# Performance work log

Hardware: AMD Instinct MI355X
Metric: run time of the kernel (lower is better)

Reference implementation:

```python
import jax, jax.numpy as jnp
import numpy as np

N = 50000
H = 256
EPS = 1e-5

def setup_inputs() -> dict:
    key = jax.random.key(0)
    ks = jax.random.split(key, 8)
    d = 128
    inp = {
        'x': jax.random.normal(ks[0], (N, d), jnp.float32),
        'edge_index': jax.random.randint(ks[1], (2, 800000), 0, N, jnp.int64),
        'W1': jax.random.normal(ks[2], (d, H), jnp.float32) * (2.0 / d) ** 0.5,
        'b1': jnp.zeros((H,), jnp.float32),
        'g1': jnp.ones((H,), jnp.float32),
        'be1': jnp.zeros((H,), jnp.float32),
        'W2': jax.random.normal(ks[3], (H, H), jnp.float32) * (2.0 / H) ** 0.5,
        'b2': jnp.zeros((H,), jnp.float32),
        'g2': jnp.ones((H,), jnp.float32),
        'be2': jnp.zeros((H,), jnp.float32),
        'W3': jax.random.normal(ks[4], (H, H), jnp.float32) * (2.0 / H) ** 0.5,
        'b3': jnp.zeros((H,), jnp.float32),
        'g3': jnp.ones((H,), jnp.float32),
        'be3': jnp.zeros((H,), jnp.float32),
        'Wf1': jax.random.normal(ks[5], (H, H // 2), jnp.float32) * (2.0 / H) ** 0.5,
        'bf1': jnp.zeros((H // 2,), jnp.float32),
        'Wf2': jax.random.normal(ks[6], (H // 2, 1), jnp.float32) * (2.0 / (H // 2)) ** 0.5,
        'bf2': jnp.zeros((1,), jnp.float32),
    }
    return inp

def _gcn_norm(edge_index):
    # add self-loops, symmetric normalization (PyG GCNConv defaults)
    loop = jnp.arange(N, dtype=edge_index.dtype)
    row = jnp.concatenate([edge_index[0], loop])  # source
    col = jnp.concatenate([edge_index[1], loop])  # target
    deg = jax.ops.segment_sum(jnp.ones_like(col, jnp.float32), col, num_segments=N)
    dis = jnp.where(deg > 0, jax.lax.rsqrt(deg), 0.0)
    norm = dis[row] * dis[col]  # [E+N]
    return row, col, norm

def _conv(x, W, b, row, col, norm):
    xw = x @ W                       # [N,H]
    msg = xw[row] * norm[:, None]    # gather + scale, [E+N,H]
    out = jax.ops.segment_sum(msg, col, num_segments=N)
    return out + b

def _ln(x, g, b):
    mu = jnp.mean(x, axis=-1, keepdims=True)
    var = jnp.var(x, axis=-1, keepdims=True)
    return (x - mu) * jax.lax.rsqrt(var + EPS) * g + b

def reference(x, edge_index, W1, b1, g1, be1, W2, b2, g2, be2, W3, b3, g3, be3, Wf1, bf1, Wf2, bf2):
    row, col, norm = _gcn_norm(edge_index)
    x1 = jax.nn.relu(_ln(_conv(x, W1, b1, row, col, norm), g1, be1))
    x2 = jax.nn.relu(_ln(_conv(x1, W2, b2, row, col, norm), g2, be2)) + 0.7 * x1
    x3 = jax.nn.relu(_ln(_conv(x2, W3, b3, row, col, norm), g3, be3)) * 0.7 + x2
    h = jax.nn.relu(x3 @ Wf1 + bf1)
    return h @ Wf2 + bf2  # [N,1]
```

## Files before the change

kernel.cpp:

```cpp
#include <hip/hip_runtime.h>
#include <cstdint>
#include <cstddef>

#define HDIM 256
#define DIN 128
#define EPSV 1e-5f
#define SCHUNK 1024

typedef __attribute__((ext_vector_type(8))) short short8;
typedef __attribute__((ext_vector_type(4))) float f32x4;

__device__ __forceinline__ float bf2f(unsigned int u16) {
  union { unsigned int i; float f; } v; v.i = u16 << 16; return v.f;
}
__device__ __forceinline__ unsigned short f2bf(float f) {
  union { float f; unsigned int i; } v; v.f = f;
  unsigned int u = v.i;
  return (unsigned short)((u + 0x7fffu + ((u >> 16) & 1u)) >> 16);
}
__device__ __forceinline__ float4 ldbf4(const unsigned short* p) {
  uint2 v = *(const uint2*)p;
  return make_float4(bf2f(v.x & 0xffffu), bf2f(v.x >> 16),
                     bf2f(v.y & 0xffffu), bf2f(v.y >> 16));
}
__device__ __forceinline__ void stbf4(unsigned short* p, float a, float b, float c, float d) {
  uint2 o;
  o.x = (unsigned int)f2bf(a) | ((unsigned int)f2bf(b) << 16);
  o.y = (unsigned int)f2bf(c) | ((unsigned int)f2bf(d) << 16);
  *(uint2*)p = o;
}
#define ACC8(u) do { \
    acc[0] += bf2f((u).x & 0xffffu); acc[1] += bf2f((u).x >> 16); \
    acc[2] += bf2f((u).y & 0xffffu); acc[3] += bf2f((u).y >> 16); \
    acc[4] += bf2f((u).z & 0xffffu); acc[5] += bf2f((u).z >> 16); \
    acc[6] += bf2f((u).w & 0xffffu); acc[7] += bf2f((u).w >> 16); } while (0)

__global__ __launch_bounds__(256) void hist_k(const int* __restrict__ col, int* deg, int e) {
  int i = blockIdx.x * 256 + threadIdx.x;
  if (i < e) atomicAdd(&deg[col[i]], 1);
}

__global__ __launch_bounds__(256) void scanA_k(const int* __restrict__ deg,
                                               int* __restrict__ row_ptr,
                                               int* __restrict__ blockSums,
                                               float* __restrict__ dis, int n) {
  __shared__ int waveSums[4];
  const int tid = threadIdx.x, lane = tid & 63, w = tid >> 6;
  const int base = blockIdx.x * SCHUNK + tid * 4;
  int v0 = 0, v1 = 0, v2 = 0, v3 = 0;
  if (base + 0 < n) v0 = deg[base + 0];
  if (base + 1 < n) v1 = deg[base + 1];
  if (base + 2 < n) v2 = deg[base + 2];
  if (base + 3 < n) v3 = deg[base + 3];
  if (base + 0 < n) dis[base + 0] = rsqrtf((float)(v0 + 1));
  if (base + 1 < n) dis[base + 1] = rsqrtf((float)(v1 + 1));
  if (base + 2 < n) dis[base + 2] = rsqrtf((float)(v2 + 1));
  if (base + 3 < n) dis[base + 3] = rsqrtf((float)(v3 + 1));
  int tsum = v0 + v1 + v2 + v3;
  int inc = tsum;
#pragma unroll
  for (int off = 1; off < 64; off <<= 1) {
    int t = __shfl_up(inc, off);
    if (lane >= off) inc += t;
  }
  if (lane == 63) waveSums[w] = inc;
  __syncthreads();
  int woff = 0;
#pragma unroll
  for (int k = 0; k < 4; ++k) woff += (k < w) ? waveSums[k] : 0;
  int excl = woff + inc - tsum;
  if (base + 0 < n) row_ptr[base + 0] = excl;
  if (base + 1 < n) row_ptr[base + 1] = excl + v0;
  if (base + 2 < n) row_ptr[base + 2] = excl + v0 + v1;
  if (base + 3 < n) row_ptr[base + 3] = excl + v0 + v1 + v2;
  if (tid == 255) blockSums[blockIdx.x] = woff + inc;
}

__global__ __launch_bounds__(256) void scanC_k(int* __restrict__ row_ptr,
                                               const int* __restrict__ bsums,
                                               int n, int e, int nbs) {
  __shared__ int s_add;
  if (threadIdx.x < 64) {
    int v = (threadIdx.x < nbs && threadIdx.x < blockIdx.x) ? bsums[threadIdx.x] : 0;
#pragma unroll
    for (int off = 1; off < 64; off <<= 1) v += __shfl_xor(v, off);
    if (threadIdx.x == 0) s_add = v;
  }
  __syncthreads();
  const int add = s_add;
  const int base = blockIdx.x * SCHUNK + threadIdx.x * 4;
#pragma unroll
  for (int k = 0; k < 4; ++k)
    if (base + k < n) row_ptr[base + k] += add;
  if (blockIdx.x == 0 && threadIdx.x == 0) row_ptr[n] = e;
}

__global__ __launch_bounds__(256) void fill_k(const int* __restrict__ row,
                                              const int* __restrict__ col,
                                              const int* __restrict__ row_ptr,
                                              int* cur, int* srcs, int e) {
  int i = blockIdx.x * 256 + threadIdx.x;
  if (i < e) {
    int c = col[i];
    int p = row_ptr[c] + atomicAdd(&cur[c], 1);
    srcs[p] = row[i];
  }
}

__device__ __forceinline__ void packW(const float* __restrict__ W,
                                      unsigned short* __restrict__ out,
                                      int idx, int C) {
  int j = idx & 7, lane = (idx >> 3) & 63, rest = idx >> 9;
  int NSUB = C >> 4;
  int ns = rest % NSUB, kb = rest / NSUB;
  int k = kb * 32 + (lane >> 4) * 8 + j;
  int c = ns * 16 + (lane & 15);
  out[idx] = f2bf(W[(size_t)k * C + c]);
}

__global__ __launch_bounds__(256) void prep_k(
    const float* __restrict__ W1, const float* __restrict__ W2,
    const float* __restrict__ W3, const float* __restrict__ Wf1,
    const float* __restrict__ x, const float* __restrict__ dis,
    unsigned short* __restrict__ W1p, unsigned short* __restrict__ W2p,
    unsigned short* __restrict__ W3p, unsigned short* __restrict__ Wf1p,
    unsigned short* __restrict__ xs, int nx) {
  int idx = blockIdx.x * 256 + threadIdx.x;
  const int s0 = DIN * HDIM, s1 = s0 + HDIM * HDIM, s2 = s1 + HDIM * HDIM,
            s3 = s2 + HDIM * 128;
  if (idx < s0) packW(W1, W1p, idx, HDIM);
  else if (idx < s1) packW(W2, W2p, idx - s0, HDIM);
  else if (idx < s2) packW(W3, W3p, idx - s1, HDIM);
  else if (idx < s3) packW(Wf1, Wf1p, idx - s2, 128);
  else {
    int o = idx - s3;
    if (o < nx) xs[o] = f2bf(x[o] * dis[o >> 7]);
  }
}

__global__ __launch_bounds__(256) void gather256_k(
    const unsigned short* __restrict__ xs, const int* __restrict__ row_ptr,
    const int* __restrict__ srcs, const float* __restrict__ dis,
    unsigned short* __restrict__ out, int n) {
  int wv = blockIdx.x * 4 + (threadIdx.x >> 6);
  int lane = threadIdx.x & 63;
  int half = lane >> 5, li = lane & 31;
  int i = wv * 2 + half;
  bool valid = i < n;
  int ic = valid ? i : n - 1;
  int beg = row_ptr[ic], end = row_ptr[ic + 1];
  float di = dis[ic];
  const int co = li * 8;
  const unsigned short* xb = xs + co;
  float acc[8];
  {
    uint4 v = *(const uint4*)(xb + (size_t)ic * 256);
    acc[0] = bf2f(v.x & 0xffffu); acc[1] = bf2f(v.x >> 16);
    acc[2] = bf2f(v.y & 0xffffu); acc[3] = bf2f(v.y >> 16);
    acc[4] = bf2f(v.z & 0xffffu); acc[5] = bf2f(v.z >> 16);
    acc[6] = bf2f(v.w & 0xffffu); acc[7] = bf2f(v.w >> 16);
  }
  int j = beg;
  for (; j + 16 <= end; j += 16) {
    int4 sA = *(const int4*)(srcs + j);
    int4 sB = *(const int4*)(srcs + j + 4);
    int4 sC = *(const int4*)(srcs + j + 8);
    int4 sD = *(const int4*)(srcs + j + 12);
    uint4 u0 = *(const uint4*)(xb + (size_t)sA.x * 256);
    uint4 u1 = *(const uint4*)(xb + (size_t)sA.y * 256);
    uint4 u2 = *(const uint4*)(xb + (size_t)sA.z * 256);
    uint4 u3 = *(const uint4*)(xb + (size_t)sA.w * 256);
    uint4 u4 = *(const uint4*)(xb + (size_t)sB.x * 256);
    uint4 u5 = *(const uint4*)(xb + (size_t)sB.y * 256);
    uint4 u6 = *(const uint4*)(xb + (size_t)sB.z * 256);
    uint4 u7 = *(const uint4*)(xb + (size_t)sB.w * 256);
    uint4 u8 = *(const uint4*)(xb + (size_t)sC.x * 256);
    uint4 u9 = *(const uint4*)(xb + (size_t)sC.y * 256);
    uint4 uA = *(const uint4*)(xb + (size_t)sC.z * 256);
    uint4 uB = *(const uint4*)(xb + (size_t)sC.w * 256);
    uint4 uC = *(const uint4*)(xb + (size_t)sD.x * 256);
    uint4 uD = *(const uint4*)(xb + (size_t)sD.y * 256);
    uint4 uE = *(const uint4*)(xb + (size_t)sD.z * 256);
    uint4 uF = *(const uint4*)(xb + (size_t)sD.w * 256);
    ACC8(u0); ACC8(u1); ACC8(u2); ACC8(u3);
    ACC8(u4); ACC8(u5); ACC8(u6); ACC8(u7);
    ACC8(u8); ACC8(u9); ACC8(uA); ACC8(uB);
    ACC8(uC); ACC8(uD); ACC8(uE); ACC8(uF);
  }
  for (; j + 4 <= end; j += 4) {
    int4 sA = *(const int4*)(srcs + j);
    uint4 u0 = *(const uint4*)(xb + (size_t)sA.x * 256);
    uint4 u1 = *(const uint4*)(xb + (size_t)sA.y * 256);
    uint4 u2 = *(const uint4*)(xb + (size_t)sA.z * 256);
    uint4 u3 = *(const uint4*)(xb + (size_t)sA.w * 256);
    ACC8(u0); ACC8(u1); ACC8(u2); ACC8(u3);
  }
  for (; j < end; ++j) {
    uint4 u = *(const uint4*)(xb + (size_t)srcs[j] * 256);
    ACC8(u);
  }
  if (valid) {
    uint4 o;
    o.x = (unsigned int)f2bf(di * acc[0]) | ((unsigned int)f2bf(di * acc[1]) << 16);
    o.y = (unsigned int)f2bf(di * acc[2]) | ((unsigned int)f2bf(di * acc[3]) << 16);
    o.z = (unsigned int)f2bf(di * acc[4]) | ((unsigned int)f2bf(di * acc[5]) << 16);
    o.w = (unsigned int)f2bf(di * acc[6]) | ((unsigned int)f2bf(di * acc[7]) << 16);
    *(uint4*)(out + (size_t)i * 256 + co) = o;
  }
}

__global__ __launch_bounds__(256) void gather128_k(
    const unsigned short* __restrict__ xs, const int* __restrict__ row_ptr,
    const int* __restrict__ srcs, const float* __restrict__ dis,
    unsigned short* __restrict__ out, int n) {
  int wv = blockIdx.x * 4 + (threadIdx.x >> 6);
  int lane = threadIdx.x & 63;
  int q = lane >> 4, li = lane & 15;
  int i = wv * 4 + q;
  bool valid = i < n;
  int ic = valid ? i : n - 1;
  int beg = row_ptr[ic], end = row_ptr[ic + 1];
  float di = dis[ic];
  const int co = li * 8;
  const unsigned short* xb = xs + co;
  float acc[8];
  {
    uint4 v = *(const uint4*)(xb + (size_t)ic * 128);
    acc[0] = bf2f(v.x & 0xffffu); acc[1] = bf2f(v.x >> 16);
    acc[2] = bf2f(v.y & 0xffffu); acc[3] = bf2f(v.y >> 16);
    acc[4] = bf2f(v.z & 0xffffu); acc[5] = bf2f(v.z >> 16);
    acc[6] = bf2f(v.w & 0xffffu); acc[7] = bf2f(v.w >> 16);
  }
  int j = beg;
  for (; j + 16 <= end; j += 16) {
    int4 sA = *(const int4*)(srcs + j);
    int4 sB = *(const int4*)(srcs + j + 4);
    int4 sC = *(const int4*)(srcs + j + 8);
    int4 sD = *(const int4*)(srcs + j + 12);
    uint4 u0 = *(const uint4*)(xb + (size_t)sA.x * 128);
    uint4 u1 = *(const uint4*)(xb + (size_t)sA.y * 128);
    uint4 u2 = *(const uint4*)(xb + (size_t)sA.z * 128);
    uint4 u3 = *(const uint4*)(xb + (size_t)sA.w * 128);
    uint4 u4 = *(const uint4*)(xb + (size_t)sB.x * 128);
    uint4 u5 = *(const uint4*)(xb + (size_t)sB.y * 128);
    uint4 u6 = *(const uint4*)(xb + (size_t)sB.z * 128);
    uint4 u7 = *(const uint4*)(xb + (size_t)sB.w * 128);
    uint4 u8 = *(const uint4*)(xb + (size_t)sC.x * 128);
    uint4 u9 = *(const uint4*)(xb + (size_t)sC.y * 128);
    uint4 uA = *(const uint4*)(xb + (size_t)sC.z * 128);
    uint4 uB = *(const uint4*)(xb + (size_t)sC.w * 128);
    uint4 uC = *(const uint4*)(xb + (size_t)sD.x * 128);
    uint4 uD = *(const uint4*)(xb + (size_t)sD.y * 128);
    uint4 uE = *(const uint4*)(xb + (size_t)sD.z * 128);
    uint4 uF = *(const uint4*)(xb + (size_t)sD.w * 128);
    ACC8(u0); ACC8(u1); ACC8(u2); ACC8(u3);
    ACC8(u4); ACC8(u5); ACC8(u6); ACC8(u7);
    ACC8(u8); ACC8(u9); ACC8(uA); ACC8(uB);
    ACC8(uC); ACC8(uD); ACC8(uE); ACC8(uF);
  }
  for (; j + 4 <= end; j += 4) {
    int4 sA = *(const int4*)(srcs + j);
    uint4 u0 = *(const uint4*)(xb + (size_t)sA.x * 128);
    uint4 u1 = *(const uint4*)(xb + (size_t)sA.y * 128);
    uint4 u2 = *(const uint4*)(xb + (size_t)sA.z * 128);
    uint4 u3 = *(const uint4*)(xb + (size_t)sA.w * 128);
    ACC8(u0); ACC8(u1); ACC8(u2); ACC8(u3);
  }
  for (; j < end; ++j) {
    uint4 u = *(const uint4*)(xb + (size_t)srcs[j] * 128);
    ACC8(u);
  }
  if (valid) {
    uint4 o;
    o.x = (unsigned int)f2bf(di * acc[0]) | ((unsigned int)f2bf(di * acc[1]) << 16);
    o.y = (unsigned int)f2bf(di * acc[2]) | ((unsigned int)f2bf(di * acc[3]) << 16);
    o.z = (unsigned int)f2bf(di * acc[4]) | ((unsigned int)f2bf(di * acc[5]) << 16);
    o.w = (unsigned int)f2bf(di * acc[6]) | ((unsigned int)f2bf(di * acc[7]) << 16);
    *(uint4*)(out + (size_t)i * 128 + co) = o;
  }
}

template<int MODE, int K, bool SOUT>
__global__ __launch_bounds__(512) void gemmln_k(
    const unsigned short* __restrict__ A, const unsigned short* __restrict__ Wp,
    const float* __restrict__ bias, const float* __restrict__ gam,
    const float* __restrict__ bet, const unsigned short* __restrict__ xprev,
    const float* __restrict__ dis, unsigned short* __restrict__ out, int n) {
  constexpr int CN = 256, NSUB = 16, KC = K / 32;
  __shared__ float red_s[64][4], red_q[64][4];
  const int t = threadIdx.x;
  const int w = t >> 6, lane = t & 63;
  const int rg = w & 1, cg = w >> 1;
  const int gq = lane >> 4, i = lane & 15;
  const int m0 = blockIdx.x * 64;
  const int r0 = m0 + rg * 32 + i, r1 = r0 + 16;
  const int l0 = r0 < n ? r0 : n - 1, l1 = r1 < n ? r1 : n - 1;
  const unsigned short* a0 = A + (size_t)l0 * K + gq * 8;
  const unsigned short* a1 = A + (size_t)l1 * K + gq * 8;
  const short8* wp = (const short8*)Wp + (size_t)(cg * 4) * 64 + lane;

  f32x4 acc[2][4];
#pragma unroll
  for (int rr = 0; rr < 2; ++rr)
#pragma unroll
    for (int j = 0; j < 4; ++j) acc[rr][j] = (f32x4){0.f, 0.f, 0.f, 0.f};

  short8 af0 = *(const short8*)a0;
  short8 af1 = *(const short8*)a1;
  short8 wf[4];
#pragma unroll
  for (int j = 0; j < 4; ++j) wf[j] = wp[j * 64];

#pragma unroll
  for (int kc = 0; kc < KC; ++kc) {
    short8 naf0, naf1, nwf[4];
    if (kc + 1 < KC) {
      naf0 = *(const short8*)(a0 + (kc + 1) * 32);
      naf1 = *(const short8*)(a1 + (kc + 1) * 32);
#pragma unroll
      for (int j = 0; j < 4; ++j) nwf[j] = wp[(size_t)(kc + 1) * NSUB * 64 + j * 64];
    }
#pragma unroll
    for (int j = 0; j < 4; ++j) {
      acc[0][j] = __builtin_amdgcn_mfma_f32_16x16x32_bf16(wf[j], af0, acc[0][j], 0, 0, 0);
      acc[1][j] = __builtin_amdgcn_mfma_f32_16x16x32_bf16(wf[j], af1, acc[1][j], 0, 0, 0);
    }
    if (kc + 1 < KC) {
      af0 = naf0; af1 = naf1;
#pragma unroll
      for (int j = 0; j < 4; ++j) wf[j] = nwf[j];
    }
  }

  const int colb = cg * 64 + gq * 4;
  float s0 = 0.f, q0 = 0.f, s1 = 0.f, q1 = 0.f;
#pragma unroll
  for (int j = 0; j < 4; ++j) {
    f32x4 b4 = *(const f32x4*)(bias + colb + j * 16);
#pragma unroll
    for (int r = 0; r < 4; ++r) {
      acc[0][j][r] += b4[r];
      acc[1][j][r] += b4[r];
      float v = acc[0][j][r]; s0 += v; q0 += v * v;
      float u = acc[1][j][r]; s1 += u; q1 += u * u;
    }
  }
  s0 += __shfl_xor(s0, 16); s0 += __shfl_xor(s0, 32);
  q0 += __shfl_xor(q0, 16); q0 += __shfl_xor(q0, 32);
  s1 += __shfl_xor(s1, 16); s1 += __shfl_xor(s1, 32);
  q1 += __shfl_xor(q1, 16); q1 += __shfl_xor(q1, 32);
  if (gq == 0) {
    red_s[rg * 32 + i][cg] = s0;      red_q[rg * 32 + i][cg] = q0;
    red_s[rg * 32 + 16 + i][cg] = s1; red_q[rg * 32 + 16 + i][cg] = q1;
  }
  __syncthreads();

#pragma unroll
  for (int rr = 0; rr < 2; ++rr) {
    int il = rg * 32 + rr * 16 + i;
    int r = m0 + il;
    if (r >= n) continue;
    float ss = (red_s[il][0] + red_s[il][1]) + (red_s[il][2] + red_s[il][3]);
    float qq = (red_q[il][0] + red_q[il][1]) + (red_q[il][2] + red_q[il][3]);
    float mu = ss * (1.f / CN);
    float inv = rsqrtf(qq * (1.f / CN) - mu * mu + EPSV);
    float di = dis[r];
    float rinv = (MODE != 0) ? 1.0f / di : 0.f;
    unsigned short* op = out + (size_t)r * CN + colb;
    const unsigned short* pp = (MODE != 0) ? (xprev + (size_t)r * CN + colb) : nullptr;
#pragma unroll
    for (int j = 0; j < 4; ++j) {
      f32x4 g4 = *(const f32x4*)(gam + colb + j * 16);
      f32x4 e4 = *(const f32x4*)(bet + colb + j * 16);
      float o0 = fmaxf((acc[rr][j][0] - mu) * inv * g4[0] + e4[0], 0.f);
      float o1 = fmaxf((acc[rr][j][1] - mu) * inv * g4[1] + e4[1], 0.f);
      float o2 = fmaxf((acc[rr][j][2] - mu) * inv * g4[2] + e4[2], 0.f);
      float o3 = fmaxf((acc[rr][j][3] - mu) * inv * g4[3] + e4[3], 0.f);
      if (MODE == 1) {
        float4 pv = ldbf4(pp + j * 16);
        o0 += 0.7f * rinv * pv.x; o1 += 0.7f * rinv * pv.y;
        o2 += 0.7f * rinv * pv.z; o3 += 0.7f * rinv * pv.w;
      } else if (MODE == 2) {
        float4 pv = ldbf4(pp + j * 16);
        o0 = o0 * 0.7f + rinv * pv.x; o1 = o1 * 0.7f + rinv * pv.y;
        o2 = o2 * 0.7f + rinv * pv.z; o3 = o3 * 0.7f + rinv * pv.w;
      }
      if (SOUT) { o0 *= di; o1 *= di; o2 *= di; o3 *= di; }
      stbf4(op + j * 16, o0, o1, o2, o3);
    }
  }
}

__global__ __launch_bounds__(256) void gemmdot_k(
    const unsigned short* __restrict__ A, const unsigned short* __restrict__ Wp,
    const float* __restrict__ b1, const float* __restrict__ w2,
    const float* __restrict__ b2, float* __restrict__ out, int n) {
  constexpr int K = 256, NSUB = 8, KC = 8;
  __shared__ float redh[64][2];
  const int t = threadIdx.x;
  const int w = t >> 6, lane = t & 63;
  const int rg = w & 1, cg = w >> 1;
  const int gq = lane >> 4, i = lane & 15;
  const int m0 = blockIdx.x * 64;
  const int r0 = m0 + rg * 32 + i, r1 = r0 + 16;
  const int l0 = r0 < n ? r0 : n - 1, l1 = r1 < n ? r1 : n - 1;
  const unsigned short* a0 = A + (size_t)l0 * K + gq * 8;
  const unsigned short* a1 = A + (size_t)l1 * K + gq * 8;
  const short8* wp = (const short8*)Wp + (size_t)(cg * 4) * 64 + lane;

  f32x4 acc[2][4];
#pragma unroll
  for (int rr = 0; rr < 2; ++rr)
#pragma unroll
    for (int j = 0; j < 4; ++j) acc[rr][j] = (f32x4){0.f, 0.f, 0.f, 0.f};

  short8 af0 = *(const short8*)a0;
  short8 af1 = *(const short8*)a1;
  short8 wf[4];
#pragma unroll
  for (int j = 0; j < 4; ++j) wf[j] = wp[j * 64];

#pragma unroll
  for (int kc = 0; kc < KC; ++kc) {
    short8 naf0, naf1, nwf[4];
    if (kc + 1 < KC) {
      naf0 = *(const short8*)(a0 + (kc + 1) * 32);
      naf1 = *(const short8*)(a1 + (kc + 1) * 32);
#pragma unroll
      for (int j = 0; j < 4; ++j) nwf[j] = wp[(size_t)(kc + 1) * NSUB * 64 + j * 64];
    }
#pragma unroll
    for (int j = 0; j < 4; ++j) {
      acc[0][j] = __builtin_amdgcn_mfma_f32_16x16x32_bf16(wf[j], af0, acc[0][j], 0, 0, 0);
      acc[1][j] = __builtin_amdgcn_mfma_f32_16x16x32_bf16(wf[j], af1, acc[1][j], 0, 0, 0);
    }
    if (kc + 1 < KC) {
      af0 = naf0; af1 = naf1;
#pragma unroll
      for (int j = 0; j < 4; ++j) wf[j] = nwf[j];
    }
  }

  const int colb = cg * 64 + gq * 4;
  float p0 = 0.f, p1 = 0.f;
#pragma unroll
  for (int j = 0; j < 4; ++j) {
    f32x4 bb = *(const f32x4*)(b1 + colb + j * 16);
    f32x4 ww = *(const f32x4*)(w2 + colb + j * 16);
#pragma unroll
    for (int r = 0; r < 4; ++r) {
      p0 += fmaxf(acc[0][j][r] + bb[r], 0.f) * ww[r];
      p1 += fmaxf(acc[1][j][r] + bb[r], 0.f) * ww[r];
    }
  }
  p0 += __shfl_xor(p0, 16); p0 += __shfl_xor(p0, 32);
  p1 += __shfl_xor(p1, 16); p1 += __shfl_xor(p1, 32);
  if (gq == 0) {
    redh[rg * 32 + i][cg] = p0;
    redh[rg * 32 + 16 + i][cg] = p1;
  }
  __syncthreads();
  if (t < 64) {
    int r = m0 + t;
    if (r < n) out[r] = redh[t][0] + redh[t][1] + b2[0];
  }
}

extern "C" void kernel_launch(void* const* d_in, const int* in_sizes, int n_in,
                              void* d_out, int out_size, void* d_ws, size_t ws_size,
                              hipStream_t stream) {
  const float* x   = (const float*)d_in[0];
  const int*   ei  = (const int*)d_in[1];
  const float* W1  = (const float*)d_in[2];
  const float* b1  = (const float*)d_in[3];
  const float* g1  = (const float*)d_in[4];
  const float* be1 = (const float*)d_in[5];
  const float* W2  = (const float*)d_in[6];
  const float* b2  = (const float*)d_in[7];
  const float* g2  = (const float*)d_in[8];
  const float* be2 = (const float*)d_in[9];
  const float* W3  = (const float*)d_in[10];
  const float* b3  = (const float*)d_in[11];
  const float* g3  = (const float*)d_in[12];
  const float* be3 = (const float*)d_in[13];
  const float* Wf1 = (const float*)d_in[14];
  const float* bf1 = (const float*)d_in[15];
  const float* Wf2 = (const float*)d_in[16];
  const float* bf2 = (const float*)d_in[17];
  float* out = (float*)d_out;

  const int n = in_sizes[0] / DIN;
  const int e = in_sizes[1] / 2;
  const int* row = ei;
  const int* col = ei + e;

  char* ws = (char*)d_ws;
  size_t off = 0;
  auto alloc = [&](size_t bytes) -> void* {
    void* p = ws + off;
    off = (off + bytes + 255) & ~(size_t)255;
    return p;
  };
  float*          dis     = (float*)alloc((size_t)n * 4);
  int*            deg_i   = (int*)alloc((size_t)n * 4);
  int*            cur     = (int*)alloc((size_t)n * 4);
  int*            row_ptr = (int*)alloc((size_t)(n + 1) * 4);
  int*            bsums   = (int*)alloc((size_t)256 * 4);
  int*            srcs    = (int*)alloc((size_t)e * 4);
  unsigned short* W1p     = (unsigned short*)alloc((size_t)DIN * HDIM * 2);
  unsigned short* W2p     = (unsigned short*)alloc((size_t)HDIM * HDIM * 2);
  unsigned short* W3p     = (unsigned short*)alloc((size_t)HDIM * HDIM * 2);
  unsigned short* Wf1p    = (unsigned short*)alloc((size_t)HDIM * 128 * 2);
  unsigned short* xsb     = (unsigned short*)alloc((size_t)n * DIN * 2);
  unsigned short* agg     = (unsigned short*)alloc((size_t)n * HDIM * 2);
  unsigned short* x1s     = (unsigned short*)alloc((size_t)n * HDIM * 2);
  unsigned short* x2s     = (unsigned short*)alloc((size_t)n * HDIM * 2);
  unsigned short* a1      = agg;
  unsigned short* x3      = x1s;

  const int eb  = (e + 255) / 256;
  const int gb  = (n + 63) / 64;
  const int sb_ = (n + SCHUNK - 1) / SCHUNK;
  const int g2b = (n + 7) / 8;
  const int g1b = (n + 15) / 16;
  const int prep_tot = DIN * HDIM + HDIM * HDIM + HDIM * HDIM + HDIM * 128 + n * DIN;

  hipMemsetAsync(deg_i, 0, ((char*)row_ptr - (char*)deg_i), stream);
  hist_k<<<eb, 256, 0, stream>>>(col, deg_i, e);
  scanA_k<<<sb_, 256, 0, stream>>>(deg_i, row_ptr, bsums, dis, n);
  scanC_k<<<sb_, 256, 0, stream>>>(row_ptr, bsums, n, e, sb_);
  fill_k<<<eb, 256, 0, stream>>>(row, col, row_ptr, cur, srcs, e);

  prep_k<<<(prep_tot + 255) / 256, 256, 0, stream>>>(W1, W2, W3, Wf1, x, dis,
                                                     W1p, W2p, W3p, Wf1p, xsb, n * DIN);

  gather128_k<<<g1b, 256, 0, stream>>>(xsb, row_ptr, srcs, dis, a1, n);
  gemmln_k<0, DIN, true><<<gb, 512, 0, stream>>>(a1, W1p, b1, g1, be1, nullptr, dis, x1s, n);

  gather256_k<<<g2b, 256, 0, stream>>>(x1s, row_ptr, srcs, dis, agg, n);
  gemmln_k<1, HDIM, true><<<gb, 512, 0, stream>>>(agg, W2p, b2, g2, be2, x1s, dis, x2s, n);

  gather256_k<<<g2b, 256, 0, stream>>>(x2s, row_ptr, srcs, dis, agg, n);
  gemmln_k<2, HDIM, false><<<gb, 512, 0, stream>>>(agg, W3p, b3, g3, be3, x2s, dis, x3, n);

  gemmdot_k<<<gb, 256, 0, stream>>>(x3, Wf1p, bf1, Wf2, bf2, out, n);
}
```

Before: 470.5 us.

## Fuse neighbor gather into GEMM+LayerNorm kernel via shared-memory tile

```diff
diff --git a/kernel.cpp b/kernel.cpp
--- a/kernel.cpp
+++ b/kernel.cpp
@@ -138,165 +138,97 @@
   }
 }
 
-__global__ __launch_bounds__(256) void gather256_k(
+template<int MODE, int K, bool SOUT>
+__global__ __launch_bounds__(512) void fused_k(
     const unsigned short* __restrict__ xs, const int* __restrict__ row_ptr,
     const int* __restrict__ srcs, const float* __restrict__ dis,
-    unsigned short* __restrict__ out, int n) {
-  int wv = blockIdx.x * 4 + (threadIdx.x >> 6);
-  int lane = threadIdx.x & 63;
-  int half = lane >> 5, li = lane & 31;
-  int i = wv * 2 + half;
-  bool valid = i < n;
-  int ic = valid ? i : n - 1;
-  int beg = row_ptr[ic], end = row_ptr[ic + 1];
-  float di = dis[ic];
-  const int co = li * 8;
-  const unsigned short* xb = xs + co;
-  float acc[8];
-  {
-    uint4 v = *(const uint4*)(xb + (size_t)ic * 256);
-    acc[0] = bf2f(v.x & 0xffffu); acc[1] = bf2f(v.x >> 16);
-    acc[2] = bf2f(v.y & 0xffffu); acc[3] = bf2f(v.y >> 16);
-    acc[4] = bf2f(v.z & 0xffffu); acc[5] = bf2f(v.z >> 16);
-    acc[6] = bf2f(v.w & 0xffffu); acc[7] = bf2f(v.w >> 16);
-  }
-  int j = beg;
-  for (; j + 16 <= end; j += 16) {
-    int4 sA = *(const int4*)(srcs + j);
-    int4 sB = *(const int4*)(srcs + j + 4);
-    int4 sC = *(const int4*)(srcs + j + 8);
-    int4 sD = *(const int4*)(srcs + j + 12);
-    uint4 u0 = *(const uint4*)(xb + (size_t)sA.x * 256);
-    uint4 u1 = *(const uint4*)(xb + (size_t)sA.y * 256);
-    uint4 u2 = *(const uint4*)(xb + (size_t)sA.z * 256);
-    uint4 u3 = *(const uint4*)(xb + (size_t)sA.w * 256);
-    uint4 u4 = *(const uint4*)(xb + (size_t)sB.x * 256);
-    uint4 u5 = *(const uint4*)(xb + (size_t)sB.y * 256);
-    uint4 u6 = *(const uint4*)(xb + (size_t)sB.z * 256);
-    uint4 u7 = *(const uint4*)(xb + (size_t)sB.w * 256);
-    uint4 u8 = *(const uint4*)(xb + (size_t)sC.x * 256);
-    uint4 u9 = *(const uint4*)(xb + (size_t)sC.y * 256);
-    uint4 uA = *(const uint4*)(xb + (size_t)sC.z * 256);
-    uint4 uB = *(const uint4*)(xb + (size_t)sC.w * 256);
-    uint4 uC = *(const uint4*)(xb + (size_t)sD.x * 256);
-    uint4 uD = *(const uint4*)(xb + (size_t)sD.y * 256);
-    uint4 uE = *(const uint4*)(xb + (size_t)sD.z * 256);
-    uint4 uF = *(const uint4*)(xb + (size_t)sD.w * 256);
-    ACC8(u0); ACC8(u1); ACC8(u2); ACC8(u3);
-    ACC8(u4); ACC8(u5); ACC8(u6); ACC8(u7);
-    ACC8(u8); ACC8(u9); ACC8(uA); ACC8(uB);
-    ACC8(uC); ACC8(uD); ACC8(uE); ACC8(uF);
-  }
-  for (; j + 4 <= end; j += 4) {
-    int4 sA = *(const int4*)(srcs + j);
-    uint4 u0 = *(const uint4*)(xb + (size_t)sA.x * 256);
-    uint4 u1 = *(const uint4*)(xb + (size_t)sA.y * 256);
-    uint4 u2 = *(const uint4*)(xb + (size_t)sA.z * 256);
-    uint4 u3 = *(const uint4*)(xb + (size_t)sA.w * 256);
-    ACC8(u0); ACC8(u1); ACC8(u2); ACC8(u3);
-  }
-  for (; j < end; ++j) {
-    uint4 u = *(const uint4*)(xb + (size_t)srcs[j] * 256);
-    ACC8(u);
-  }
-  if (valid) {
-    uint4 o;
-    o.x = (unsigned int)f2bf(di * acc[0]) | ((unsigned int)f2bf(di * acc[1]) << 16);
-    o.y = (unsigned int)f2bf(di * acc[2]) | ((unsigned int)f2bf(di * acc[3]) << 16);
-    o.z = (unsigned int)f2bf(di * acc[4]) | ((unsigned int)f2bf(di * acc[5]) << 16);
-    o.w = (unsigned int)f2bf(di * acc[6]) | ((unsigned int)f2bf(di * acc[7]) << 16);
-    *(uint4*)(out + (size_t)i * 256 + co) = o;
-  }
-}
-
-__global__ __launch_bounds__(256) void gather128_k(
-    const unsigned short* __restrict__ xs, const int* __restrict__ row_ptr,
-    const int* __restrict__ srcs, const float* __restrict__ dis,
-    unsigned short* __restrict__ out, int n) {
-  int wv = blockIdx.x * 4 + (threadIdx.x >> 6);
-  int lane = threadIdx.x & 63;
-  int q = lane >> 4, li = lane & 15;
-  int i = wv * 4 + q;
-  bool valid = i < n;
-  int ic = valid ? i : n - 1;
-  int beg = row_ptr[ic], end = row_ptr[ic + 1];
-  float di = dis[ic];
-  const int co = li * 8;
-  const unsigned short* xb = xs + co;
-  float acc[8];
-  {
-    uint4 v = *(const uint4*)(xb + (size_t)ic * 128);
-    acc[0] = bf2f(v.x & 0xffffu); acc[1] = bf2f(v.x >> 16);
-    acc[2] = bf2f(v.y & 0xffffu); acc[3] = bf2f(v.y >> 16);
-    acc[4] = bf2f(v.z & 0xffffu); acc[5] = bf2f(v.z >> 16);
-    acc[6] = bf2f(v.w & 0xffffu); acc[7] = bf2f(v.w >> 16);
-  }
-  int j = beg;
-  for (; j + 16 <= end; j += 16) {
-    int4 sA = *(const int4*)(srcs + j);
-    int4 sB = *(const int4*)(srcs + j + 4);
-    int4 sC = *(const int4*)(srcs + j + 8);
-    int4 sD = *(const int4*)(srcs + j + 12);
-    uint4 u0 = *(const uint4*)(xb + (size_t)sA.x * 128);
-    uint4 u1 = *(const uint4*)(xb + (size_t)sA.y * 128);
-    uint4 u2 = *(const uint4*)(xb + (size_t)sA.z * 128);
-    uint4 u3 = *(const uint4*)(xb + (size_t)sA.w * 128);
-    uint4 u4 = *(const uint4*)(xb + (size_t)sB.x * 128);
-    uint4 u5 = *(const uint4*)(xb + (size_t)sB.y * 128);
-    uint4 u6 = *(const uint4*)(xb + (size_t)sB.z * 128);
-    uint4 u7 = *(const uint4*)(xb + (size_t)sB.w * 128);
-    uint4 u8 = *(const uint4*)(xb + (size_t)sC.x * 128);
-    uint4 u9 = *(const uint4*)(xb + (size_t)sC.y * 128);
-    uint4 uA = *(const uint4*)(xb + (size_t)sC.z * 128);
-    uint4 uB = *(const uint4*)(xb + (size_t)sC.w * 128);
-    uint4 uC = *(const uint4*)(xb + (size_t)sD.x * 128);
-    uint4 uD = *(const uint4*)(xb + (size_t)sD.y * 128);
-    uint4 uE = *(const uint4*)(xb + (size_t)sD.z * 128);
-    uint4 uF = *(const uint4*)(xb + (size_t)sD.w * 128);
-    ACC8(u0); ACC8(u1); ACC8(u2); ACC8(u3);
-    ACC8(u4); ACC8(u5); ACC8(u6); ACC8(u7);
-    ACC8(u8); ACC8(u9); ACC8(uA); ACC8(uB);
-    ACC8(uC); ACC8(uD); ACC8(uE); ACC8(uF);
-  }
-  for (; j + 4 <= end; j += 4) {
-    int4 sA = *(const int4*)(srcs + j);
-    uint4 u0 = *(const uint4*)(xb + (size_t)sA.x * 128);
-    uint4 u1 = *(const uint4*)(xb + (size_t)sA.y * 128);
-    uint4 u2 = *(const uint4*)(xb + (size_t)sA.z * 128);
-    uint4 u3 = *(const uint4*)(xb + (size_t)sA.w * 128);
-    ACC8(u0); ACC8(u1); ACC8(u2); ACC8(u3);
-  }
-  for (; j < end; ++j) {
-    uint4 u = *(const uint4*)(xb + (size_t)srcs[j] * 128);
-    ACC8(u);
-  }
-  if (valid) {
-    uint4 o;
-    o.x = (unsigned int)f2bf(di * acc[0]) | ((unsigned int)f2bf(di * acc[1]) << 16);
-    o.y = (unsigned int)f2bf(di * acc[2]) | ((unsigned int)f2bf(di * acc[3]) << 16);
-    o.z = (unsigned int)f2bf(di * acc[4]) | ((unsigned int)f2bf(di * acc[5]) << 16);
-    o.w = (unsigned int)f2bf(di * acc[6]) | ((unsigned int)f2bf(di * acc[7]) << 16);
-    *(uint4*)(out + (size_t)i * 128 + co) = o;
-  }
-}
-
-template<int MODE, int K, bool SOUT>
-__global__ __launch_bounds__(512) void gemmln_k(
-    const unsigned short* __restrict__ A, const unsigned short* __restrict__ Wp,
+    const unsigned short* __restrict__ Wp,
     const float* __restrict__ bias, const float* __restrict__ gam,
     const float* __restrict__ bet, const unsigned short* __restrict__ xprev,
-    const float* __restrict__ dis, unsigned short* __restrict__ out, int n) {
+    unsigned short* __restrict__ out, int n) {
   constexpr int CN = 256, NSUB = 16, KC = K / 32;
+  constexpr int STRIDE = K + 8;
+  constexpr int LPR = K / 8;
+  constexpr int RP = 64 / LPR;
+  constexpr int NIT = 8 / RP;
+  __shared__ unsigned short aggS[64 * STRIDE];
   __shared__ float red_s[64][4], red_q[64][4];
+
   const int t = threadIdx.x;
   const int w = t >> 6, lane = t & 63;
+  const int m0 = blockIdx.x * 64;
+
+  {
+    const int gi = lane / LPR, li = lane % LPR;
+    const unsigned short* xb = xs + li * 8;
+#pragma unroll
+    for (int it = 0; it < NIT; ++it) {
+      const int lr = w * 8 + it * RP + gi;
+      const int tg = m0 + lr;
+      const int tgc = tg < n ? tg : n - 1;
+      const int beg = row_ptr[tgc], end = row_ptr[tgc + 1];
+      const float di = dis[tgc];
+      float acc[8];
+      {
+        uint4 v = *(const uint4*)(xb + (size_t)tgc * K);
+        acc[0] = bf2f(v.x & 0xffffu); acc[1] = bf2f(v.x >> 16);
+        acc[2] = bf2f(v.y & 0xffffu); acc[3] = bf2f(v.y >> 16);
+        acc[4] = bf2f(v.z & 0xffffu); acc[5] = bf2f(v.z >> 16);
+        acc[6] = bf2f(v.w & 0xffffu); acc[7] = bf2f(v.w >> 16);
+      }
+      int j = beg;
+      for (; j + 16 <= end; j += 16) {
+        int4 sA = *(const int4*)(srcs + j);
+        int4 sB = *(const int4*)(srcs + j + 4);
+        int4 sC = *(const int4*)(srcs + j + 8);
+        int4 sD = *(const int4*)(srcs + j + 12);
+        uint4 u0 = *(const uint4*)(xb + (size_t)sA.x * K);
+        uint4 u1 = *(const uint4*)(xb + (size_t)sA.y * K);
+        uint4 u2 = *(const uint4*)(xb + (size_t)sA.z * K);
+        uint4 u3 = *(const uint4*)(xb + (size_t)sA.w * K);
+        uint4 u4 = *(const uint4*)(xb + (size_t)sB.x * K);
+        uint4 u5 = *(const uint4*)(xb + (size_t)sB.y * K);
+        uint4 u6 = *(const uint4*)(xb + (size_t)sB.z * K);
+        uint4 u7 = *(const uint4*)(xb + (size_t)sB.w * K);
+        uint4 u8 = *(const uint4*)(xb + (size_t)sC.x * K);
+        uint4 u9 = *(const uint4*)(xb + (size_t)sC.y * K);
+        uint4 uA = *(const uint4*)(xb + (size_t)sC.z * K);
+        uint4 uB = *(const uint4*)(xb + (size_t)sC.w * K);
+        uint4 uC = *(const uint4*)(xb + (size_t)sD.x * K);
+        uint4 uD = *(const uint4*)(xb + (size_t)sD.y * K);
+        uint4 uE = *(const uint4*)(xb + (size_t)sD.z * K);
+        uint4 uF = *(const uint4*)(xb + (size_t)sD.w * K);
+        ACC8(u0); ACC8(u1); ACC8(u2); ACC8(u3);
+        ACC8(u4); ACC8(u5); ACC8(u6); ACC8(u7);
+        ACC8(u8); ACC8(u9); ACC8(uA); ACC8(uB);
+        ACC8(uC); ACC8(uD); ACC8(uE); ACC8(uF);
+      }
+      for (; j + 4 <= end; j += 4) {
+        int4 sA = *(const int4*)(srcs + j);
+        uint4 u0 = *(const uint4*)(xb + (size_t)sA.x * K);
+        uint4 u1 = *(const uint4*)(xb + (size_t)sA.y * K);
+        uint4 u2 = *(const uint4*)(xb + (size_t)sA.z * K);
+        uint4 u3 = *(const uint4*)(xb + (size_t)sA.w * K);
+        ACC8(u0); ACC8(u1); ACC8(u2); ACC8(u3);
+      }
+      for (; j < end; ++j) {
+        uint4 u = *(const uint4*)(xb + (size_t)srcs[j] * K);
+        ACC8(u);
+      }
+      uint4 o;
+      o.x = (unsigned int)f2bf(di * acc[0]) | ((unsigned int)f2bf(di * acc[1]) << 16);
+      o.y = (unsigned int)f2bf(di * acc[2]) | ((unsigned int)f2bf(di * acc[3]) << 16);
+      o.z = (unsigned int)f2bf(di * acc[4]) | ((unsigned int)f2bf(di * acc[5]) << 16);
+      o.w = (unsigned int)f2bf(di * acc[6]) | ((unsigned int)f2bf(di * acc[7]) << 16);
+      *(uint4*)&aggS[lr * STRIDE + li * 8] = o;
+    }
+  }
+  __syncthreads();
+
   const int rg = w & 1, cg = w >> 1;
   const int gq = lane >> 4, i = lane & 15;
-  const int m0 = blockIdx.x * 64;
-  const int r0 = m0 + rg * 32 + i, r1 = r0 + 16;
-  const int l0 = r0 < n ? r0 : n - 1, l1 = r1 < n ? r1 : n - 1;
-  const unsigned short* a0 = A + (size_t)l0 * K + gq * 8;
-  const unsigned short* a1 = A + (size_t)l1 * K + gq * 8;
+  const unsigned short* aL0 = &aggS[(rg * 32 + i) * STRIDE + gq * 8];
+  const unsigned short* aL1 = aL0 + 16 * STRIDE;
   const short8* wp = (const short8*)Wp + (size_t)(cg * 4) * 64 + lane;
 
   f32x4 acc[2][4];
@@ -305,28 +237,25 @@
 #pragma unroll
     for (int j = 0; j < 4; ++j) acc[rr][j] = (f32x4){0.f, 0.f, 0.f, 0.f};
 
-  short8 af0 = *(const short8*)a0;
-  short8 af1 = *(const short8*)a1;
   short8 wf[4];
 #pragma unroll
   for (int j = 0; j < 4; ++j) wf[j] = wp[j * 64];
 
 #pragma unroll
   for (int kc = 0; kc < KC; ++kc) {
-    short8 naf0, naf1, nwf[4];
+    short8 nwf[4];
     if (kc + 1 < KC) {
-      naf0 = *(const short8*)(a0 + (kc + 1) * 32);
-      naf1 = *(const short8*)(a1 + (kc + 1) * 32);
 #pragma unroll
       for (int j = 0; j < 4; ++j) nwf[j] = wp[(size_t)(kc + 1) * NSUB * 64 + j * 64];
     }
+    short8 af0 = *(const short8*)(aL0 + kc * 32);
+    short8 af1 = *(const short8*)(aL1 + kc * 32);
 #pragma unroll
     for (int j = 0; j < 4; ++j) {
       acc[0][j] = __builtin_amdgcn_mfma_f32_16x16x32_bf16(wf[j], af0, acc[0][j], 0, 0, 0);
       acc[1][j] = __builtin_amdgcn_mfma_f32_16x16x32_bf16(wf[j], af1, acc[1][j], 0, 0, 0);
     }
     if (kc + 1 < KC) {
-      af0 = naf0; af1 = naf1;
 #pragma unroll
       for (int j = 0; j < 4; ++j) wf[j] = nwf[j];
     }
@@ -512,17 +441,13 @@
   unsigned short* W3p     = (unsigned short*)alloc((size_t)HDIM * HDIM * 2);
   unsigned short* Wf1p    = (unsigned short*)alloc((size_t)HDIM * 128 * 2);
   unsigned short* xsb     = (unsigned short*)alloc((size_t)n * DIN * 2);
-  unsigned short* agg     = (unsigned short*)alloc((size_t)n * HDIM * 2);
   unsigned short* x1s     = (unsigned short*)alloc((size_t)n * HDIM * 2);
   unsigned short* x2s     = (unsigned short*)alloc((size_t)n * HDIM * 2);
-  unsigned short* a1      = agg;
-  unsigned short* x3      = x1s;
+  unsigned short* x3      = (unsigned short*)alloc((size_t)n * HDIM * 2);
 
   const int eb  = (e + 255) / 256;
   const int gb  = (n + 63) / 64;
   const int sb_ = (n + SCHUNK - 1) / SCHUNK;
-  const int g2b = (n + 7) / 8;
-  const int g1b = (n + 15) / 16;
   const int prep_tot = DIN * HDIM + HDIM * HDIM + HDIM * HDIM + HDIM * 128 + n * DIN;
 
   hipMemsetAsync(deg_i, 0, ((char*)row_ptr - (char*)deg_i), stream);
@@ -534,14 +459,14 @@
   prep_k<<<(prep_tot + 255) / 256, 256, 0, stream>>>(W1, W2, W3, Wf1, x, dis,
                                                      W1p, W2p, W3p, Wf1p, xsb, n * DIN);
 
-  gather128_k<<<g1b, 256, 0, stream>>>(xsb, row_ptr, srcs, dis, a1, n);
-  gemmln_k<0, DIN, true><<<gb, 512, 0, stream>>>(a1, W1p, b1, g1, be1, nullptr, dis, x1s, n);
-
-  gather256_k<<<g2b, 256, 0, stream>>>(x1s, row_ptr, srcs, dis, agg, n);
-  gemmln_k<1, HDIM, true><<<gb, 512, 0, stream>>>(agg, W2p, b2, g2, be2, x1s, dis, x2s, n);
-
-  gather256_k<<<g2b, 256, 0, stream>>>(x2s, row_ptr, srcs, dis, agg, n);
-  gemmln_k<2, HDIM, false><<<gb, 512, 0, stream>>>(agg, W3p, b3, g3, be3, x2s, dis, x3, n);
+  fused_k<0, DIN, true><<<gb, 512, 0, stream>>>(
+      xsb, row_ptr, srcs, dis, W1p, b1, g1, be1, nullptr, x1s, n);
+
+  fused_k<1, HDIM, true><<<gb, 512, 0, stream>>>(
+      x1s, row_ptr, srcs, dis, W2p, b2, g2, be2, x1s, x2s, n);
+
+  fused_k<2, HDIM, false><<<gb, 512, 0, stream>>>(
+      x2s, row_ptr, srcs, dis, W3p, b3, g3, be3, x2s, x3, n);
 
   gemmdot_k<<<gb, 256, 0, stream>>>(x3, Wf1p, bf1, Wf2, bf2, out, n);
 }
```

After: 480.4 us. +2.1%, slower.

## Widen GEMM tiles to 128 rows and record atomic ranks in CSR build

Applied to the files above, without the earlier changes.

```diff
diff --git a/kernel.cpp b/kernel.cpp
--- a/kernel.cpp
+++ b/kernel.cpp
@@ -35,9 +35,10 @@
     acc[4] += bf2f((u).z & 0xffffu); acc[5] += bf2f((u).z >> 16); \
     acc[6] += bf2f((u).w & 0xffffu); acc[7] += bf2f((u).w >> 16); } while (0)
 
-__global__ __launch_bounds__(256) void hist_k(const int* __restrict__ col, int* deg, int e) {
+__global__ __launch_bounds__(256) void hist_k(const int* __restrict__ col,
+                                              int* deg, int* __restrict__ rank, int e) {
   int i = blockIdx.x * 256 + threadIdx.x;
-  if (i < e) atomicAdd(&deg[col[i]], 1);
+  if (i < e) rank[i] = atomicAdd(&deg[col[i]], 1);
 }
 
 __global__ __launch_bounds__(256) void scanA_k(const int* __restrict__ deg,
@@ -98,13 +99,10 @@
 __global__ __launch_bounds__(256) void fill_k(const int* __restrict__ row,
                                               const int* __restrict__ col,
                                               const int* __restrict__ row_ptr,
-                                              int* cur, int* srcs, int e) {
+                                              const int* __restrict__ rank,
+                                              int* __restrict__ srcs, int e) {
   int i = blockIdx.x * 256 + threadIdx.x;
-  if (i < e) {
-    int c = col[i];
-    int p = row_ptr[c] + atomicAdd(&cur[c], 1);
-    srcs[p] = row[i];
-  }
+  if (i < e) srcs[row_ptr[col[i]] + rank[i]] = row[i];
 }
 
 __device__ __forceinline__ void packW(const float* __restrict__ W,
@@ -286,56 +284,56 @@
     const float* __restrict__ bias, const float* __restrict__ gam,
     const float* __restrict__ bet, const unsigned short* __restrict__ xprev,
     const float* __restrict__ dis, unsigned short* __restrict__ out, int n) {
-  constexpr int CN = 256, NSUB = 16, KC = K / 32;
-  __shared__ float red_s[64][4], red_q[64][4];
+  constexpr int CN = 256, NSUBT = 16, KC = K / 32;
+  __shared__ float red_s[128][2], red_q[128][2];
   const int t = threadIdx.x;
   const int w = t >> 6, lane = t & 63;
-  const int rg = w & 1, cg = w >> 1;
+  const int rg = w & 3, cg = w >> 2;
   const int gq = lane >> 4, i = lane & 15;
-  const int m0 = blockIdx.x * 64;
+  const int m0 = blockIdx.x * 128;
   const int r0 = m0 + rg * 32 + i, r1 = r0 + 16;
   const int l0 = r0 < n ? r0 : n - 1, l1 = r1 < n ? r1 : n - 1;
   const unsigned short* a0 = A + (size_t)l0 * K + gq * 8;
   const unsigned short* a1 = A + (size_t)l1 * K + gq * 8;
-  const short8* wp = (const short8*)Wp + (size_t)(cg * 4) * 64 + lane;
-
-  f32x4 acc[2][4];
+  const short8* wp = (const short8*)Wp + (size_t)(cg * 8) * 64 + lane;
+
+  f32x4 acc[2][8];
 #pragma unroll
   for (int rr = 0; rr < 2; ++rr)
 #pragma unroll
-    for (int j = 0; j < 4; ++j) acc[rr][j] = (f32x4){0.f, 0.f, 0.f, 0.f};
+    for (int j = 0; j < 8; ++j) acc[rr][j] = (f32x4){0.f, 0.f, 0.f, 0.f};
 
   short8 af0 = *(const short8*)a0;
   short8 af1 = *(const short8*)a1;
-  short8 wf[4];
-#pragma unroll
-  for (int j = 0; j < 4; ++j) wf[j] = wp[j * 64];
+  short8 wf[8];
+#pragma unroll
+  for (int j = 0; j < 8; ++j) wf[j] = wp[j * 64];
 
 #pragma unroll
   for (int kc = 0; kc < KC; ++kc) {
-    short8 naf0, naf1, nwf[4];
+    short8 naf0, naf1, nwf[8];
     if (kc + 1 < KC) {
       naf0 = *(const short8*)(a0 + (kc + 1) * 32);
       naf1 = *(const short8*)(a1 + (kc + 1) * 32);
 #pragma unroll
-      for (int j = 0; j < 4; ++j) nwf[j] = wp[(size_t)(kc + 1) * NSUB * 64 + j * 64];
-    }
-#pragma unroll
-    for (int j = 0; j < 4; ++j) {
+      for (int j = 0; j < 8; ++j) nwf[j] = wp[(size_t)(kc + 1) * NSUBT * 64 + j * 64];
+    }
+#pragma unroll
+    for (int j = 0; j < 8; ++j) {
       acc[0][j] = __builtin_amdgcn_mfma_f32_16x16x32_bf16(wf[j], af0, acc[0][j], 0, 0, 0);
       acc[1][j] = __builtin_amdgcn_mfma_f32_16x16x32_bf16(wf[j], af1, acc[1][j], 0, 0, 0);
     }
     if (kc + 1 < KC) {
       af0 = naf0; af1 = naf1;
 #pragma unroll
-      for (int j = 0; j < 4; ++j) wf[j] = nwf[j];
-    }
-  }
-
-  const int colb = cg * 64 + gq * 4;
+      for (int j = 0; j < 8; ++j) wf[j] = nwf[j];
+    }
+  }
+
+  const int colb = cg * 128 + gq * 4;
   float s0 = 0.f, q0 = 0.f, s1 = 0.f, q1 = 0.f;
 #pragma unroll
-  for (int j = 0; j < 4; ++j) {
+  for (int j = 0; j < 8; ++j) {
     f32x4 b4 = *(const f32x4*)(bias + colb + j * 16);
 #pragma unroll
     for (int r = 0; r < 4; ++r) {
@@ -360,8 +358,8 @@
     int il = rg * 32 + rr * 16 + i;
     int r = m0 + il;
     if (r >= n) continue;
-    float ss = (red_s[il][0] + red_s[il][1]) + (red_s[il][2] + red_s[il][3]);
-    float qq = (red_q[il][0] + red_q[il][1]) + (red_q[il][2] + red_q[il][3]);
+    float ss = red_s[il][0] + red_s[il][1];
+    float qq = red_q[il][0] + red_q[il][1];
     float mu = ss * (1.f / CN);
     float inv = rsqrtf(qq * (1.f / CN) - mu * mu + EPSV);
     float di = dis[r];
@@ -369,7 +367,7 @@
     unsigned short* op = out + (size_t)r * CN + colb;
     const unsigned short* pp = (MODE != 0) ? (xprev + (size_t)r * CN + colb) : nullptr;
 #pragma unroll
-    for (int j = 0; j < 4; ++j) {
+    for (int j = 0; j < 8; ++j) {
       f32x4 g4 = *(const f32x4*)(gam + colb + j * 16);
       f32x4 e4 = *(const f32x4*)(bet + colb + j * 16);
       float o0 = fmaxf((acc[rr][j][0] - mu) * inv * g4[0] + e4[0], 0.f);
@@ -391,17 +389,17 @@
   }
 }
 
-__global__ __launch_bounds__(256) void gemmdot_k(
+__global__ __launch_bounds__(512) void gemmdot_k(
     const unsigned short* __restrict__ A, const unsigned short* __restrict__ Wp,
     const float* __restrict__ b1, const float* __restrict__ w2,
     const float* __restrict__ b2, float* __restrict__ out, int n) {
-  constexpr int K = 256, NSUB = 8, KC = 8;
-  __shared__ float redh[64][2];
+  constexpr int K = 256, NSUBT = 8, KC = 8;
+  __shared__ float redh[128][2];
   const int t = threadIdx.x;
   const int w = t >> 6, lane = t & 63;
-  const int rg = w & 1, cg = w >> 1;
+  const int rg = w & 3, cg = w >> 2;
   const int gq = lane >> 4, i = lane & 15;
-  const int m0 = blockIdx.x * 64;
+  const int m0 = blockIdx.x * 128;
   const int r0 = m0 + rg * 32 + i, r1 = r0 + 16;
   const int l0 = r0 < n ? r0 : n - 1, l1 = r1 < n ? r1 : n - 1;
   const unsigned short* a0 = A + (size_t)l0 * K + gq * 8;
@@ -427,7 +425,7 @@
       naf0 = *(const short8*)(a0 + (kc + 1) * 32);
       naf1 = *(const short8*)(a1 + (kc + 1) * 32);
 #pragma unroll
-      for (int j = 0; j < 4; ++j) nwf[j] = wp[(size_t)(kc + 1) * NSUB * 64 + j * 64];
+      for (int j = 0; j < 4; ++j) nwf[j] = wp[(size_t)(kc + 1) * NSUBT * 64 + j * 64];
     }
 #pragma unroll
     for (int j = 0; j < 4; ++j) {
@@ -460,7 +458,7 @@
     redh[rg * 32 + 16 + i][cg] = p1;
   }
   __syncthreads();
-  if (t < 64) {
+  if (t < 128) {
     int r = m0 + t;
     if (r < n) out[r] = redh[t][0] + redh[t][1] + b2[0];
   }
@@ -503,9 +501,9 @@
   };
   float*          dis     = (float*)alloc((size_t)n * 4);
   int*            deg_i   = (int*)alloc((size_t)n * 4);
-  int*            cur     = (int*)alloc((size_t)n * 4);
   int*            row_ptr = (int*)alloc((size_t)(n + 1) * 4);
   int*            bsums   = (int*)alloc((size_t)256 * 4);
+  int*            rank    = (int*)alloc((size_t)e * 4);
   int*            srcs    = (int*)alloc((size_t)e * 4);
   unsigned short* W1p     = (unsigned short*)alloc((size_t)DIN * HDIM * 2);
   unsigned short* W2p     = (unsigned short*)alloc((size_t)HDIM * HDIM * 2);
@@ -519,17 +517,17 @@
   unsigned short* x3      = x1s;
 
   const int eb  = (e + 255) / 256;
-  const int gb  = (n + 63) / 64;
+  const int gb  = (n + 127) / 128;
   const int sb_ = (n + SCHUNK - 1) / SCHUNK;
   const int g2b = (n + 7) / 8;
   const int g1b = (n + 15) / 16;
   const int prep_tot = DIN * HDIM + HDIM * HDIM + HDIM * HDIM + HDIM * 128 + n * DIN;
 
-  hipMemsetAsync(deg_i, 0, ((char*)row_ptr - (char*)deg_i), stream);
-  hist_k<<<eb, 256, 0, stream>>>(col, deg_i, e);
+  hipMemsetAsync(deg_i, 0, (size_t)n * 4, stream);
+  hist_k<<<eb, 256, 0, stream>>>(col, deg_i, rank, e);
   scanA_k<<<sb_, 256, 0, stream>>>(deg_i, row_ptr, bsums, dis, n);
   scanC_k<<<sb_, 256, 0, stream>>>(row_ptr, bsums, n, e, sb_);
-  fill_k<<<eb, 256, 0, stream>>>(row, col, row_ptr, cur, srcs, e);
+  fill_k<<<eb, 256, 0, stream>>>(row, col, row_ptr, rank, srcs, e);
 
   prep_k<<<(prep_tot + 255) / 256, 256, 0, stream>>>(W1, W2, W3, Wf1, x, dis,
                                                      W1p, W2p, W3p, Wf1p, xsb, n * DIN);
@@ -543,5 +541,5 @@
   gather256_k<<<g2b, 256, 0, stream>>>(x2s, row_ptr, srcs, dis, agg, n);
   gemmln_k<2, HDIM, false><<<gb, 512, 0, stream>>>(agg, W3p, b3, g3, be3, x2s, dis, x3, n);
 
-  gemmdot_k<<<gb, 256, 0, stream>>>(x3, Wf1p, bf1, Wf2, bf2, out, n);
-}
+  gemmdot_k<<<gb, 512, 0, stream>>>(x3, Wf1p, bf1, Wf2, bf2, out, n);
+}
```

After: 427.0 us (median of 2 runs). 9.3% less time.
